# Performance work log

Measured on AMD Instinct MI355X. Metric: run time of the kernel, lower is better.

The kernel has to match this reference:

```python
import jax, jax.numpy as jnp
import numpy as np
from jax import lax

N, D, K = 131072, 128, 1024
BETA = 1.0
EMA_DECAY = 0.85

def setup_inputs() -> dict:
    key = jax.random.key(0)
    k1, k2, k3, k4 = jax.random.split(key, 4)
    return {
        "x": jax.random.normal(k1, (N, D), dtype=jnp.float32),
        "embeddings": jax.random.uniform(k2, (D, K), dtype=jnp.float32),
        "ema_count": jax.random.uniform(k3, (K,), dtype=jnp.float32),
        "embeddings_sum": jax.random.uniform(k4, (D, K), dtype=jnp.float32),
    }

def reference(x, embeddings, ema_count, embeddings_sum):
    input_shape = x.shape
    flat = x.reshape(-1, D)                      # [N, D]
    # squared-euclidean distances via expanded ||a-b||^2
    sim = flat @ embeddings                      # [N, K]
    dist = (jnp.sum(flat ** 2, axis=1, keepdims=True)
            + jnp.sum(embeddings ** 2, axis=0)
            - 2.0 * sim)                         # [N, K]
    idx = jnp.argmin(dist, axis=1)               # [N] int
    # codebook lookup (gather instead of one-hot matmul)
    quantized = jnp.take(embeddings.T, idx, axis=0).reshape(input_shape)
    # EMA update (segment_sum instead of one-hot matmul scatter)
    count = jax.ops.segment_sum(jnp.ones((flat.shape[0],), flat.dtype), idx,
                                num_segments=K)                  # [K]
    ema_count_new = (1.0 - EMA_DECAY) * ema_count + EMA_DECAY * count
    sums = jax.ops.segment_sum(flat, idx, num_segments=K).T      # [D, K]
    embeddings_sum_new = (1.0 - EMA_DECAY) * embeddings_sum + EMA_DECAY * sums
    embeddings_new = embeddings_sum_new / jnp.maximum(ema_count_new, 1e-5)
    # losses (commitment added via add_loss in original)
    commitment_loss = jnp.mean((lax.stop_gradient(quantized) - x) ** 2)
    # straight-through estimator
    q_st = x + lax.stop_gradient(quantized - x)
    return q_st, embeddings_new, ema_count_new, embeddings_sum_new, BETA * commitment_loss
```

## Files before the change

kernel.cpp:

```cpp
#include <hip/hip_runtime.h>
#include <cfloat>
#include <cstdint>

#define NROWS 131072
#define DIMD  128
#define KCODE 1024
#define MARGIN 0.045f
#define RCAP  65536

typedef __attribute__((ext_vector_type(8))) _Float16 half8;
typedef __attribute__((ext_vector_type(4))) float f32x4;

union U4H8 { uint4 u; half8 h; };

#define WS_REFINE_CNT 0
#define WS_LOSS       8
#define WS_COUNTS     16
#define WS_SUMS       4608
#define WS_LPART      528896
#define WS_CURSOR     532992
#define WS_E2         537088
#define WS_ZERO_BYTES 541184
#define WS_ET         541184
#define WS_BHI        1065472
#define WS_BEST       1327616
#define WS_IDX        1589760
#define WS_ROWLIST    2114048
#define WS_REFINE     2638336
#define WS_PARTIALS   3162624

#define OUT_QST  ((size_t)0)
#define OUT_EMB  ((size_t)NROWS * DIMD)
#define OUT_CNT  (OUT_EMB + (size_t)DIMD * KCODE)
#define OUT_ES   (OUT_CNT + KCODE)
#define OUT_LOSS (OUT_ES + (size_t)DIMD * KCODE)

__device__ __forceinline__ unsigned f16pair(float a, float b) {
    union { _Float16 h[2]; unsigned u; } p;
    p.h[0] = (_Float16)a;
    p.h[1] = (_Float16)b;
    return p.u;
}

__global__ void vq_prep(const float* __restrict__ E, uint4* __restrict__ Bh,
                        float* __restrict__ ET, float* __restrict__ e2) {
    int gid = blockIdx.x * 256 + threadIdx.x;
    int l = gid & 63;
    int t = (gid >> 6) & 3;
    int NB = gid >> 8;
    int n = NB * 16 + (l & 15);
    int k0 = t * 32 + (l >> 4) * 8;
    float v[8];
    float ss = 0.f;
    #pragma unroll
    for (int j = 0; j < 8; ++j) {
        v[j] = E[(size_t)(k0 + j) * KCODE + n];
        ss = fmaf(v[j], v[j], ss);
    }
    Bh[gid] = make_uint4(f16pair(v[0], v[1]), f16pair(v[2], v[3]),
                         f16pair(v[4], v[5]), f16pair(v[6], v[7]));
    float4* et4 = (float4*)(ET + (size_t)n * DIMD + k0);
    et4[0] = make_float4(v[0], v[1], v[2], v[3]);
    et4[1] = make_float4(v[4], v[5], v[6], v[7]);
    atomicAdd(&e2[n], ss);
}


#define LOADB(bARR, ev_, nb_)                                     \
  { _Pragma("unroll")                                             \
    for (int t_ = 0; t_ < 4; ++t_)                                \
      bARR[t_] = Bh[((nb_) * 4 + t_) * 64 + l];                   \
    ev_ = e2[(nb_) * 16 + m]; }

#define COMPUTE_NB(nb_, bARR, ev_)                                           \
  {                                                                          \
    f32x4 acc[2];                                                            \
    _Pragma("unroll")                                                        \
    for (int mt_ = 0; mt_ < 2; ++mt_) acc[mt_] = (f32x4){0.f,0.f,0.f,0.f};   \
    _Pragma("unroll")                                                        \
    for (int t_ = 0; t_ < 4; ++t_) {                                         \
      U4H8 bh_; bh_.u = bARR[t_];                                            \
      _Pragma("unroll")                                                      \
      for (int mt_ = 0; mt_ < 2; ++mt_)                                      \
        acc[mt_] = __builtin_amdgcn_mfma_f32_16x16x32_f16(ah[mt_][t_], bh_.h,\
                                                          acc[mt_], 0, 0, 0);\
    }                                                                        \
    int col_ = (nb_) * 16 + m;                                               \
    _Pragma("unroll")                                                        \
    for (int mt_ = 0; mt_ < 2; ++mt_)                                        \
      _Pragma("unroll")                                                      \
      for (int r_ = 0; r_ < 4; ++r_) {                                       \
        float s_ = fmaf(-2.0f, acc[mt_][r_], ev_);                           \
        if (s_ < m1[mt_][r_]) {                                              \
          m2[mt_][r_] = m1[mt_][r_]; i2[mt_][r_] = i1[mt_][r_];              \
          m1[mt_][r_] = s_;          i1[mt_][r_] = col_;                     \
        } else if (s_ < m2[mt_][r_]) {                                       \
          m2[mt_][r_] = s_;          i2[mt_][r_] = col_;                     \
        }                                                                    \
      }                                                                      \
  }

__global__ __launch_bounds__(256, 2) void vq_argmin_mfma(
        const float* __restrict__ x, const uint4* __restrict__ Bh,
        const float* __restrict__ e2,
        int* __restrict__ idx, int* __restrict__ counts,
        int* __restrict__ refine_pairs, int* __restrict__ refine_cnt) {

    __shared__ int hist[KCODE];

    const int tid = threadIdx.x;
    const int w = tid >> 6, l = tid & 63;
    const int m = l & 15, q = l >> 4;
    const int rw = blockIdx.x * 128 + w * 32;

    uint4 bA[4], bB[4];
    float evA, evB;
    LOADB(bA, evA, 0);
    LOADB(bB, evB, 1);

    const float4* x4 = (const float4*)x;
    half8 ah[2][4];
    #pragma unroll
    for (int mt = 0; mt < 2; ++mt) {
        int row = rw + mt * 16 + m;
        #pragma unroll
        for (int t = 0; t < 4; ++t) {
            int c4 = t * 8 + q * 2;
            float4 va = x4[(size_t)row * 32 + c4];
            float4 vb = x4[(size_t)row * 32 + c4 + 1];
            half8 hh;
            hh[0] = (_Float16)va.x; hh[1] = (_Float16)va.y;
            hh[2] = (_Float16)va.z; hh[3] = (_Float16)va.w;
            hh[4] = (_Float16)vb.x; hh[5] = (_Float16)vb.y;
            hh[6] = (_Float16)vb.z; hh[7] = (_Float16)vb.w;
            ah[mt][t] = hh;
        }
    }

    float m1[2][4], m2[2][4];
    int i1[2][4], i2[2][4];
    #pragma unroll
    for (int a = 0; a < 2; ++a)
        #pragma unroll
        for (int r = 0; r < 4; ++r) {
            m1[a][r] = FLT_MAX; m2[a][r] = FLT_MAX;
            i1[a][r] = 0; i2[a][r] = 0;
        }

    for (int nb = 0; nb < 64; nb += 2) {
        COMPUTE_NB(nb, bA, evA);
        { int p = (nb + 2 <= 63) ? nb + 2 : 62; LOADB(bA, evA, p); }
        COMPUTE_NB(nb + 1, bB, evB);
        { int p = (nb + 3 <= 63) ? nb + 3 : 63; LOADB(bB, evB, p); }
    }

    #pragma unroll
    for (int mt = 0; mt < 2; ++mt)
        #pragma unroll
        for (int r = 0; r < 4; ++r) {
            float a1 = m1[mt][r], a2 = m2[mt][r];
            int ai1 = i1[mt][r], ai2 = i2[mt][r];
            #pragma unroll
            for (int off = 1; off < 16; off <<= 1) {
                float o1 = __shfl_xor(a1, off, 64);
                float o2 = __shfl_xor(a2, off, 64);
                int oi1 = __shfl_xor(ai1, off, 64);
                int oi2 = __shfl_xor(ai2, off, 64);
                bool take = (o1 < a1) || (o1 == a1 && oi1 < ai1);
                float w1 = take ? o1 : a1;  int wi1 = take ? oi1 : ai1;
                float l1 = take ? a1 : o1;  int li1 = take ? ai1 : oi1;
                float c2 = a2; int ci2 = ai2;
                if (o2 < c2 || (o2 == c2 && oi2 < ci2)) { c2 = o2; ci2 = oi2; }
                if (l1 < c2 || (l1 == c2 && li1 < ci2)) { c2 = l1; ci2 = li1; }
                a1 = w1; ai1 = wi1; a2 = c2; ai2 = ci2;
            }
            m1[mt][r] = a1; m2[mt][r] = a2;
            i1[mt][r] = ai1; i2[mt][r] = ai2;
        }

    for (int i = tid; i < KCODE; i += 256) hist[i] = 0;
    __syncthreads();
    if (m == 0) {
        #pragma unroll
        for (int mt = 0; mt < 2; ++mt)
            #pragma unroll
            for (int r = 0; r < 4; ++r) {
                int row = rw + mt * 16 + q * 4 + r;
                int bi = i1[mt][r];
                idx[row] = bi;
                atomicAdd(&hist[bi], 1);
                if (!(m2[mt][r] - m1[mt][r] > MARGIN)) {
                    int pos = atomicAdd(refine_cnt, 1);
                    if (pos < RCAP) {
                        refine_pairs[2 * pos]     = row;
                        refine_pairs[2 * pos + 1] = i2[mt][r];
                    }
                }
            }
    }
    __syncthreads();
    for (int i = tid; i < KCODE; i += 256) {
        int h = hist[i];
        if (h) atomicAdd(&counts[i], h);
    }
}

__global__ __launch_bounds__(256) void vq_refine2(
        const float* __restrict__ x, const float* __restrict__ ET,
        const float* __restrict__ e2,
        const int* __restrict__ refine_pairs, const int* __restrict__ refine_cnt,
        int* __restrict__ idx, int* __restrict__ counts) {
    int cnt = *refine_cnt;
    if (cnt > RCAP) cnt = RCAP;
    for (int e = blockIdx.x * 256 + threadIdx.x; e < cnt; e += gridDim.x * 256) {
        int n  = refine_pairs[2 * e];
        int kb = refine_pairs[2 * e + 1];
        int ka = idx[n];
        const float4* xa = (const float4*)(x + (size_t)n * DIMD);
        const float4* ea = (const float4*)(ET + (size_t)ka * DIMD);
        const float4* eb = (const float4*)(ET + (size_t)kb * DIMD);
        float da = 0.f, db = 0.f;
        #pragma unroll 8
        for (int d4 = 0; d4 < DIMD / 4; ++d4) {
            float4 xv = xa[d4];
            float4 av = ea[d4];
            float4 bv = eb[d4];
            da = fmaf(xv.x, av.x, da); da = fmaf(xv.y, av.y, da);
            da = fmaf(xv.z, av.z, da); da = fmaf(xv.w, av.w, da);
            db = fmaf(xv.x, bv.x, db); db = fmaf(xv.y, bv.y, db);
            db = fmaf(xv.z, bv.z, db); db = fmaf(xv.w, bv.w, db);
        }
        float sa = fmaf(-2.0f, da, e2[ka]);
        float sb = fmaf(-2.0f, db, e2[kb]);
        bool swap = (sb < sa) || (sb == sa && kb < ka);
        if (swap) {
            idx[n] = kb;
            atomicSub(&counts[ka], 1);
            atomicAdd(&counts[kb], 1);
        }
    }
}

__global__ void vq_scan(const int* __restrict__ counts, int* __restrict__ cursor) {
    __shared__ int s[KCODE];
    int t = threadIdx.x;
    int c = counts[t];
    s[t] = c;
    __syncthreads();
    for (int off = 1; off < KCODE; off <<= 1) {
        int v = (t >= off) ? s[t - off] : 0;
        __syncthreads();
        s[t] += v;
        __syncthreads();
    }
    cursor[t] = s[t] - c;
}

__global__ void vq_fill(const int* __restrict__ idx, int* __restrict__ cursor,
                        int* __restrict__ rowlist) {
    __shared__ int hcnt[KCODE];
    __shared__ int hbase[KCODE];
    int tid = threadIdx.x;
    for (int i = tid; i < KCODE; i += 256) hcnt[i] = 0;
    __syncthreads();
    int n = blockIdx.x * 256 + tid;
    int k = idx[n];
    int lrank = atomicAdd(&hcnt[k], 1);
    __syncthreads();
    for (int i = tid; i < KCODE; i += 256) {
        int h = hcnt[i];
        if (h) hbase[i] = atomicAdd(&cursor[i], h);
    }
    __syncthreads();
    rowlist[hbase[k] + lrank] = n;
}

__global__ void vq_chunksum(const float* __restrict__ x,
                            const int* __restrict__ rowlist,
                            const int* __restrict__ idx,
                            const float* __restrict__ ET,
                            float* __restrict__ sums,
                            float* __restrict__ out,
                            float* __restrict__ lpart) {
    __shared__ int rl[128];
    __shared__ int kk[128];
    __shared__ float wsum[2];
    int tid = threadIdx.x;
    int base = blockIdx.x * 128;
    int r = rowlist[base + tid];
    rl[tid] = r;
    kk[tid] = idx[r];
    __syncthreads();
    float s = 0.f, lossp = 0.f;
    int kprev = kk[0];
    float qreg = ET[(size_t)kprev * DIMD + tid];
    #pragma unroll 4
    for (int j = 0; j < 128; ++j) {
        int kj = kk[j];
        if (kj != kprev) {
            atomicAdd(&sums[(size_t)kprev * DIMD + tid], s);
            s = 0.f;
            kprev = kj;
            qreg = ET[(size_t)kj * DIMD + tid];
        }
        size_t off = (size_t)rl[j] * DIMD + tid;
        float xv = x[off];
        s += xv;
        float diff = qreg - xv;
        out[OUT_QST + off] = xv + diff;
        lossp = fmaf(diff, diff, lossp);
    }
    atomicAdd(&sums[(size_t)kprev * DIMD + tid], s);
    #pragma unroll
    for (int off = 32; off > 0; off >>= 1)
        lossp += __shfl_down(lossp, off);
    if ((tid & 63) == 0) wsum[tid >> 6] = lossp;
    __syncthreads();
    if (tid == 0)
        atomicAdd(&lpart[blockIdx.x & 255], wsum[0] + wsum[1]);
}

__global__ void vq_finalize_emb(const int* __restrict__ counts,
                                const float* __restrict__ sums,
                                const float* __restrict__ emc,
                                const float* __restrict__ es,
                                const float* __restrict__ lpart,
                                float* __restrict__ out) {
    int gid = blockIdx.x * 256 + threadIdx.x;
    int k = gid & (KCODE - 1), d = gid >> 10;
    float cnt = (float)counts[k];
    float ecn = fmaf(0.85f, cnt, 0.15f * emc[k]);
    float esn = fmaf(0.85f, sums[(size_t)k * DIMD + d], 0.15f * es[(size_t)d * KCODE + k]);
    out[OUT_ES + (size_t)d * KCODE + k] = esn;
    out[OUT_EMB + (size_t)d * KCODE + k] = esn / fmaxf(ecn, 1e-5f);
    if (d == 0) out[OUT_CNT + k] = ecn;
    if (blockIdx.x == 0) {
        float v = lpart[threadIdx.x];
        #pragma unroll
        for (int off = 32; off > 0; off >>= 1)
            v += __shfl_down(v, off);
        __shared__ float ws4[4];
        if ((threadIdx.x & 63) == 0) ws4[threadIdx.x >> 6] = v;
        __syncthreads();
        if (threadIdx.x == 0)
            out[OUT_LOSS] = (ws4[0] + ws4[1] + ws4[2] + ws4[3]) /
                            ((float)NROWS * (float)DIMD);
    }
}

extern "C" void kernel_launch(void* const* d_in, const int* in_sizes, int n_in,
                              void* d_out, int out_size, void* d_ws, size_t ws_size,
                              hipStream_t stream) {
    const float* x   = (const float*)d_in[0];
    const float* E   = (const float*)d_in[1];
    const float* emc = (const float*)d_in[2];
    const float* es  = (const float*)d_in[3];
    float* out = (float*)d_out;
    char* ws = (char*)d_ws;

    int*    refine_cnt  = (int*)(ws + WS_REFINE_CNT);
    int*    counts      = (int*)(ws + WS_COUNTS);
    float*  sums        = (float*)(ws + WS_SUMS);
    float*  lpart       = (float*)(ws + WS_LPART);
    int*    cursor      = (int*)(ws + WS_CURSOR);
    float*  e2          = (float*)(ws + WS_E2);
    float*  ET          = (float*)(ws + WS_ET);
    uint4*  Bh          = (uint4*)(ws + WS_BHI);
    int*    idx         = (int*)(ws + WS_IDX);
    int*    rowlist     = (int*)(ws + WS_ROWLIST);
    int*    refine_pairs= (int*)(ws + WS_REFINE);

    hipMemsetAsync(ws, 0, WS_ZERO_BYTES, stream);

    vq_prep<<<64, 256, 0, stream>>>(E, Bh, ET, e2);
    vq_argmin_mfma<<<NROWS / 128, 256, 0, stream>>>(x, Bh, e2, idx, counts,
                                                    refine_pairs, refine_cnt);
    vq_refine2<<<256, 256, 0, stream>>>(x, ET, e2, refine_pairs, refine_cnt,
                                        idx, counts);
    vq_scan<<<1, KCODE, 0, stream>>>(counts, cursor);
    vq_fill<<<NROWS / 256, 256, 0, stream>>>(idx, cursor, rowlist);
    vq_chunksum<<<NROWS / 128, 128, 0, stream>>>(x, rowlist, idx, ET, sums,
                                                 out, lpart);
    vq_finalize_emb<<<(DIMD * KCODE) / 256, 256, 0, stream>>>(counts, sums, emc, es, lpart, out);
}
```

Before: 279.8 us.

## Split codebook across waves and pack distance+index into sortable uint keys

The argmin kernel now splits the 1024 codes between two wave pairs per block. Each wave scans half the codebook for 32 rows, the block covers 64 rows, and the grid doubles. Partial top-2 results are merged through shared memory. The running top-2 tracking replaces float compare-and-branch with packed unsigned keys: distance plus 512 keeps the value positive so its bit pattern orders like an integer, and the low 6 mantissa bits hold the column-block index, so the update is branchless min/max. The truncated mantissa bits lose some precision, which the refine margin is expected to absorb. Extra cost comes from the LDS merge, and half the waves sit idle during the final reduction.

After: 293.7 us. 5.0% more time.

```diff
diff --git a/kernel.cpp b/kernel.cpp
--- a/kernel.cpp
+++ b/kernel.cpp
@@ -70,7 +70,7 @@
   { _Pragma("unroll")                                             \
     for (int t_ = 0; t_ < 4; ++t_)                                \
       bARR[t_] = Bh[((nb_) * 4 + t_) * 64 + l];                   \
-    ev_ = e2[(nb_) * 16 + m]; }
+    ev_ = e2[(nb_) * 16 + m] + 512.0f; }
 
 #define COMPUTE_NB(nb_, bARR, ev_)                                           \
   {                                                                          \
@@ -85,18 +85,16 @@
         acc[mt_] = __builtin_amdgcn_mfma_f32_16x16x32_f16(ah[mt_][t_], bh_.h,\
                                                           acc[mt_], 0, 0, 0);\
     }                                                                        \
-    int col_ = (nb_) * 16 + m;                                               \
+    unsigned nb6_ = (unsigned)(nb_);                                         \
     _Pragma("unroll")                                                        \
     for (int mt_ = 0; mt_ < 2; ++mt_)                                        \
       _Pragma("unroll")                                                      \
       for (int r_ = 0; r_ < 4; ++r_) {                                       \
         float s_ = fmaf(-2.0f, acc[mt_][r_], ev_);                           \
-        if (s_ < m1[mt_][r_]) {                                              \
-          m2[mt_][r_] = m1[mt_][r_]; i2[mt_][r_] = i1[mt_][r_];              \
-          m1[mt_][r_] = s_;          i1[mt_][r_] = col_;                     \
-        } else if (s_ < m2[mt_][r_]) {                                       \
-          m2[mt_][r_] = s_;          i2[mt_][r_] = col_;                     \
-        }                                                                    \
+        unsigned kb_ = (__float_as_uint(s_) & 0xFFFFFFC0u) | nb6_;           \
+        unsigned hi_ = (k1[mt_][r_] > kb_) ? k1[mt_][r_] : kb_;              \
+        k1[mt_][r_] = (k1[mt_][r_] < kb_) ? k1[mt_][r_] : kb_;               \
+        k2[mt_][r_] = (k2[mt_][r_] < hi_) ? k2[mt_][r_] : hi_;               \
       }                                                                      \
   }
 
@@ -106,17 +104,21 @@
         int* __restrict__ idx, int* __restrict__ counts,
         int* __restrict__ refine_pairs, int* __restrict__ refine_cnt) {
 
+    __shared__ unsigned lk1[2][8][64];
+    __shared__ unsigned lk2[2][8][64];
     __shared__ int hist[KCODE];
 
     const int tid = threadIdx.x;
     const int w = tid >> 6, l = tid & 63;
+    const int rg = w & 1, kh = w >> 1;
     const int m = l & 15, q = l >> 4;
-    const int rw = blockIdx.x * 128 + w * 32;
+    const int rw = blockIdx.x * 64 + rg * 32;
+    const int kb0 = kh * 32;
 
     uint4 bA[4], bB[4];
     float evA, evB;
-    LOADB(bA, evA, 0);
-    LOADB(bB, evB, 1);
+    LOADB(bA, evA, kb0);
+    LOADB(bB, evB, kb0 + 1);
 
     const float4* x4 = (const float4*)x;
     half8 ah[2][4];
@@ -137,66 +139,102 @@
         }
     }
 
-    float m1[2][4], m2[2][4];
-    int i1[2][4], i2[2][4];
+    unsigned k1[2][4], k2[2][4];
     #pragma unroll
     for (int a = 0; a < 2; ++a)
         #pragma unroll
-        for (int r = 0; r < 4; ++r) {
-            m1[a][r] = FLT_MAX; m2[a][r] = FLT_MAX;
-            i1[a][r] = 0; i2[a][r] = 0;
-        }
-
-    for (int nb = 0; nb < 64; nb += 2) {
+        for (int r = 0; r < 4; ++r) { k1[a][r] = 0xFFFFFFFFu; k2[a][r] = 0xFFFFFFFFu; }
+
+    for (int ii = 0; ii < 32; ii += 2) {
+        int nb = kb0 + ii;
         COMPUTE_NB(nb, bA, evA);
-        { int p = (nb + 2 <= 63) ? nb + 2 : 62; LOADB(bA, evA, p); }
+        { int p = (ii + 2 < 32) ? nb + 2 : kb0 + 30; LOADB(bA, evA, p); }
         COMPUTE_NB(nb + 1, bB, evB);
-        { int p = (nb + 3 <= 63) ? nb + 3 : 63; LOADB(bB, evB, p); }
-    }
-
-    #pragma unroll
-    for (int mt = 0; mt < 2; ++mt)
-        #pragma unroll
-        for (int r = 0; r < 4; ++r) {
-            float a1 = m1[mt][r], a2 = m2[mt][r];
-            int ai1 = i1[mt][r], ai2 = i2[mt][r];
-            #pragma unroll
-            for (int off = 1; off < 16; off <<= 1) {
-                float o1 = __shfl_xor(a1, off, 64);
-                float o2 = __shfl_xor(a2, off, 64);
-                int oi1 = __shfl_xor(ai1, off, 64);
-                int oi2 = __shfl_xor(ai2, off, 64);
-                bool take = (o1 < a1) || (o1 == a1 && oi1 < ai1);
-                float w1 = take ? o1 : a1;  int wi1 = take ? oi1 : ai1;
-                float l1 = take ? a1 : o1;  int li1 = take ? ai1 : oi1;
-                float c2 = a2; int ci2 = ai2;
-                if (o2 < c2 || (o2 == c2 && oi2 < ci2)) { c2 = o2; ci2 = oi2; }
-                if (l1 < c2 || (l1 == c2 && li1 < ci2)) { c2 = l1; ci2 = li1; }
-                a1 = w1; ai1 = wi1; a2 = c2; ai2 = ci2;
-            }
-            m1[mt][r] = a1; m2[mt][r] = a2;
-            i1[mt][r] = ai1; i2[mt][r] = ai2;
-        }
+        { int p = (ii + 3 < 32) ? nb + 3 : kb0 + 31; LOADB(bB, evB, p); }
+    }
 
     for (int i = tid; i < KCODE; i += 256) hist[i] = 0;
-    __syncthreads();
-    if (m == 0) {
+    if (kh == 1) {
         #pragma unroll
         for (int mt = 0; mt < 2; ++mt)
             #pragma unroll
             for (int r = 0; r < 4; ++r) {
-                int row = rw + mt * 16 + q * 4 + r;
-                int bi = i1[mt][r];
-                idx[row] = bi;
-                atomicAdd(&hist[bi], 1);
-                if (!(m2[mt][r] - m1[mt][r] > MARGIN)) {
-                    int pos = atomicAdd(refine_cnt, 1);
-                    if (pos < RCAP) {
-                        refine_pairs[2 * pos]     = row;
-                        refine_pairs[2 * pos + 1] = i2[mt][r];
+                lk1[rg][mt * 4 + r][l] = k1[mt][r];
+                lk2[rg][mt * 4 + r][l] = k2[mt][r];
+            }
+    }
+    __syncthreads();
+
+    if (kh == 0) {
+        #pragma unroll
+        for (int mt = 0; mt < 2; ++mt)
+            #pragma unroll
+            for (int r = 0; r < 4; ++r) {
+                unsigned b1 = lk1[rg][mt * 4 + r][l];
+                unsigned b2 = lk2[rg][mt * 4 + r][l];
+                unsigned a1 = k1[mt][r], a2 = k2[mt][r];
+                unsigned lo = (a1 < b1) ? a1 : b1;
+                unsigned hi = (a1 < b1) ? b1 : a1;
+                unsigned m2c = (a2 < b2) ? a2 : b2;
+                k1[mt][r] = lo;
+                k2[mt][r] = (hi < m2c) ? hi : m2c;
+            }
+
+        float m1f[2][4], m2f[2][4];
+        int i1c[2][4], i2c[2][4];
+        #pragma unroll
+        for (int mt = 0; mt < 2; ++mt)
+            #pragma unroll
+            for (int r = 0; r < 4; ++r) {
+                unsigned K1 = k1[mt][r], K2 = k2[mt][r];
+                m1f[mt][r] = __uint_as_float(K1 & 0xFFFFFFC0u) - 512.0f;
+                m2f[mt][r] = __uint_as_float(K2 & 0xFFFFFFC0u) - 512.0f;
+                i1c[mt][r] = (int)(K1 & 63u) * 16 + m;
+                i2c[mt][r] = (int)(K2 & 63u) * 16 + m;
+            }
+
+        #pragma unroll
+        for (int mt = 0; mt < 2; ++mt)
+            #pragma unroll
+            for (int r = 0; r < 4; ++r) {
+                float a1 = m1f[mt][r], a2 = m2f[mt][r];
+                int ai1 = i1c[mt][r], ai2 = i2c[mt][r];
+                #pragma unroll
+                for (int off = 1; off < 16; off <<= 1) {
+                    float o1 = __shfl_xor(a1, off, 64);
+                    float o2 = __shfl_xor(a2, off, 64);
+                    int oi1 = __shfl_xor(ai1, off, 64);
+                    int oi2 = __shfl_xor(ai2, off, 64);
+                    bool take = (o1 < a1) || (o1 == a1 && oi1 < ai1);
+                    float w1 = take ? o1 : a1;  int wi1 = take ? oi1 : ai1;
+                    float l1 = take ? a1 : o1;  int li1 = take ? ai1 : oi1;
+                    float c2 = a2; int ci2 = ai2;
+                    if (o2 < c2 || (o2 == c2 && oi2 < ci2)) { c2 = o2; ci2 = oi2; }
+                    if (l1 < c2 || (l1 == c2 && li1 < ci2)) { c2 = l1; ci2 = li1; }
+                    a1 = w1; ai1 = wi1; a2 = c2; ai2 = ci2;
+                }
+                m1f[mt][r] = a1; m2f[mt][r] = a2;
+                i1c[mt][r] = ai1; i2c[mt][r] = ai2;
+            }
+
+        if (m == 0) {
+            #pragma unroll
+            for (int mt = 0; mt < 2; ++mt)
+                #pragma unroll
+                for (int r = 0; r < 4; ++r) {
+                    int row = rw + mt * 16 + q * 4 + r;
+                    int bi = i1c[mt][r];
+                    idx[row] = bi;
+                    atomicAdd(&hist[bi], 1);
+                    if (!(m2f[mt][r] - m1f[mt][r] > MARGIN)) {
+                        int pos = atomicAdd(refine_cnt, 1);
+                        if (pos < RCAP) {
+                            refine_pairs[2 * pos]     = row;
+                            refine_pairs[2 * pos + 1] = i2c[mt][r];
+                        }
                     }
                 }
-            }
+        }
     }
     __syncthreads();
     for (int i = tid; i < KCODE; i += 256) {
@@ -373,8 +411,8 @@
     hipMemsetAsync(ws, 0, WS_ZERO_BYTES, stream);
 
     vq_prep<<<64, 256, 0, stream>>>(E, Bh, ET, e2);
-    vq_argmin_mfma<<<NROWS / 128, 256, 0, stream>>>(x, Bh, e2, idx, counts,
-                                                    refine_pairs, refine_cnt);
+    vq_argmin_mfma<<<NROWS / 64, 256, 0, stream>>>(x, Bh, e2, idx, counts,
+                                                   refine_pairs, refine_cnt);
     vq_refine2<<<256, 256, 0, stream>>>(x, ET, e2, refine_pairs, refine_cnt,
                                         idx, counts);
     vq_scan<<<1, KCODE, 0, stream>>>(counts, cursor);
```
